# Performance work log

Hardware: AMD Instinct MI355X
Metric: run time of the kernel (lower is better)

Reference implementation:

```python
import jax, jax.numpy as jnp
import numpy as np

E = 1024; H = 16; D = E // H; L = 16
B = 4; TB = 1024; TW = 512
SCALE = D ** -0.5


def _rel_matrix(S):
    r = jnp.arange(S)
    return jnp.clip(r[None, :] - r[:, None], -L, L) + L  # [S,S] ints in [0, 2L]


def _heads(x):
    # [T, b, E] -> [b*H, T, D]
    T, b, _ = x.shape
    return x.reshape(T, b * H, D).transpose(1, 0, 2)


def _rel_logits(q, table, S):
    # Shaw-style relative-key logits without materializing [S,S,D] embeddings:
    # q: [n, S, D], table: [2L+1, D] -> [n, S, S]
    mat = _rel_matrix(S)                          # [S, S]
    all_r = jnp.einsum('ntd,rd->ntr', q, table)   # [n, S, 2L+1]
    return jnp.take_along_axis(all_r, mat[None, :, :], axis=2)


def setup_inputs() -> dict:
    key = jax.random.key(0)
    ks = jax.random.split(key, 10)
    s = 0.02
    w = lambda k, shape: jax.random.normal(k, shape, jnp.float32) * s
    return {
        'query_bpe': jax.random.normal(ks[0], (TB, B, E), jnp.float32),
        'query_word': jax.random.normal(ks[1], (TW, B, E), jnp.float32),
        'mapping': jax.random.uniform(ks[2], (B, TB, TW), jnp.float32),
        'Wq_bpe': w(ks[3], (E, E)), 'bq_bpe': jnp.zeros((E,), jnp.float32),
        'Wk_bpe': w(ks[4], (E, E)), 'bk_bpe': jnp.zeros((E,), jnp.float32),
        'Wq_word': w(ks[5], (E, E)), 'bq_word': jnp.zeros((E,), jnp.float32),
        'Wk_word': w(ks[6], (E, E)), 'bk_word': jnp.zeros((E,), jnp.float32),
        'Wv': w(ks[7], (E, E)), 'bv': jnp.zeros((E,), jnp.float32),
        'Wo': w(ks[8], (E, E)), 'bo': jnp.zeros((E,), jnp.float32),
        'rel_keys_bpe': w(ks[9], (2 * L + 1, D)),
    }


def reference(query_bpe, query_word, mapping, Wq_bpe, bq_bpe, Wk_bpe, bk_bpe,
              Wq_word, bq_word, Wk_word, bk_word, Wv, bv, Wo, bo, rel_keys_bpe):
    b = query_bpe.shape[1]
    q_bpe = _heads((query_bpe @ Wq_bpe.T + bq_bpe) * SCALE)    # [bH, TB, D]
    k_bpe = _heads(query_bpe @ Wk_bpe.T + bk_bpe)
    q_word = _heads((query_word @ Wq_word.T + bq_word) * SCALE)  # [bH, TW, D]
    k_word = _heads(query_word @ Wk_word.T + bk_word)
    v = _heads(query_bpe @ Wv.T + bv)
    # content + relative-position logits for both streams
    # (k_only path in source looks up relative_position_keys_bpe for BOTH streams)
    attn_bpe = q_bpe @ k_bpe.transpose(0, 2, 1) + _rel_logits(q_bpe, rel_keys_bpe, TB)
    attn_word = q_word @ k_word.transpose(0, 2, 1) + _rel_logits(q_word, rel_keys_bpe, TW)
    aw = attn_word.reshape(b, H, TW, TW)
    # fuse word-level scores into BPE positions via alignment mapping: M A M^T
    fused = jnp.einsum('bqw,bhws->bhqs', mapping, aw)
    fused = jnp.einsum('bhqs,bks->bhqk', fused, mapping)
    attn = attn_bpe.reshape(b, H, TB, TB) + fused
    probs = jax.nn.softmax(attn, axis=-1)
    out = jnp.einsum('bhqk,bhkd->bhqd', probs, v.reshape(b, H, TB, D))
    out = out.transpose(2, 0, 1, 3).reshape(TB, b, E)  # back to [T, B, E]
    return out @ Wo.T + bo
```

## Files before the change

kernel.cpp:

```cpp
#include <hip/hip_runtime.h>


#define DEV __device__ __forceinline__
#define GAS(x) ((const __attribute__((address_space(1))) unsigned*)(x))
#define LAS(x) ((__attribute__((address_space(3))) unsigned*)(x))

typedef unsigned short u16;
typedef __attribute__((ext_vector_type(8))) short short8;
typedef __attribute__((ext_vector_type(8))) _Float16 half8;
typedef __attribute__((ext_vector_type(4))) float floatx4;

DEV float bf2f(u16 u) { union { unsigned u; float f; } v; v.u = ((unsigned)u) << 16; return v.f; }
DEV u16 f2bf(float f) {
  union { float f; unsigned u; } v; v.f = f;
  unsigned r = v.u + 0x7FFFu + ((v.u >> 16) & 1u);
  return (u16)(r >> 16);
}
DEV u16 f2h_bits(float f) { union { _Float16 h; u16 u; } v; v.h = (_Float16)f; return v.u; }

template <int N> DEV void vmwait() {
  asm volatile("s_waitcnt vmcnt(%0)" ::"n"(N) : "memory");
  __builtin_amdgcn_sched_barrier(0);
}
DEV void barrier_raw() {
// ... 117 lines not shown
  if (i >= a.n8[z]) return;
  const float* s = a.src[z] + (size_t)i * 8;
  union { short8 v; u16 u[8]; } o;
#pragma unroll
  for (int j = 0; j < 8; ++j) o.u[j] = f2bf(s[j]);
  *(short8*)(a.dst[z] + (size_t)i * 8) = o.v;
}

struct CvtS { const float* src[3]; u16* dh[3]; u16* dl[3]; int n8[3]; };
__global__ __launch_bounds__(256) void cvt_split_kernel(CvtS a) {
  int z = blockIdx.z;
  int i = blockIdx.x * 256 + threadIdx.x;
  if (i >= a.n8[z]) return;
  const float* s = a.src[z] + (size_t)i * 8;
  union { short8 v; u16 u[8]; } oh, ol;
#pragma unroll
  for (int j = 0; j < 8; ++j) {
    float f = s[j];
    u16 h = f2bf(f);
    oh.u[j] = h;
    ol.u[j] = f2bf(f - bf2f(h));
  }
  *(short8*)(a.dh[z] + (size_t)i * 8) = oh.v;
  *(short8*)(a.dl[z] + (size_t)i * 8) = ol.v;
}

struct PAll {
  const float* Xf[5]; const float* Wf[5];
  const u16* Xh[5]; const u16* Xl[5]; const u16* Wh[5]; const u16* Wl[5];
  const float* bias[5]; float scale[5];
  u16* dh[5]; u16* dl[5]; int T[5]; int md[5]; int prep;
};

__global__ __launch_bounds__(256) void proj_all_kernel(PAll a) {
  const int z = blockIdx.z;
  const int T = a.T[z];
  if ((int)blockIdx.y >= (T >> 5)) return;
  __shared__ __align__(16) u16 LB[8][4096];
  const int tid = threadIdx.x;
  const int lane = tid & 63, wv = tid >> 6, wr = wv >> 1, wc = wv & 1;
  const int m = lane & 15, quad = lane >> 4;
  const int md = a.md[z], prep = a.prep;
  const int bx = blockIdx.x, by = blockIdx.y;
  const size_t arow = (size_t)by * 128 * 1024;
  const size_t brow = (size_t)bx * 128 * 1024;
  floatx4 acc[4][4];
  acc_zero(acc);
  if (prep) {
    const u16* Xh = a.Xh[z]; const u16* Xl = a.Xl[z];
    const u16* Wh = a.Wh[z]; const u16* Wl = a.Wl[z];
    if (md == 2) {
      stage_u16(Xh + arow, 1024, LB[0], tid);
      stage_u16(Wh + brow, 1024, LB[1], tid);
      stage_u16(Xl + arow, 1024, LB[2], tid);
      stage_u16(Wl + brow, 1024, LB[3], tid);
      for (int k0 = 0; k0 < 1024; k0 += 32) {
        int o = ((k0 >> 5) & 1) * 4;
        if (k0 + 32 < 1024) {
          int no = 4 - o;
          stage_u16(Xh + arow + k0 + 32, 1024, LB[no], tid);
          stage_u16(Wh + brow + k0 + 32, 1024, LB[no + 1], tid);
          stage_u16(Xl + arow + k0 + 32, 1024, LB[no + 2], tid);
          stage_u16(Wl + brow + k0 + 32, 1024, LB[no + 3], tid);
          vmwait<8>();
        } else vmwait<0>();
        barrier_raw();
        mma_split(LB[o], LB[o + 2], LB[o + 1], LB[o + 3], wr, wc, m, quad, acc);
        barrier_raw();
      }
    } else {
      stage_u16(Xh + arow, 1024, LB[0], tid);
      stage_u16(Wh + brow, 1024, LB[1], tid);
      for (int k0 = 0; k0 < 1024; k0 += 32) {
        int o = ((k0 >> 5) & 1) * 2;
        if (k0 + 32 < 1024) {
          int no = 2 - o;
          stage_u16(Xh + arow + k0 + 32, 1024, LB[no], tid);
          stage_u16(Wh + brow + k0 + 32, 1024, LB[no + 1], tid);
          vmwait<4>();
        } else vmwait<0>();
        barrier_raw();
        mma_bf16(LB[o], LB[o + 1], wr, wc, m, quad, acc);
        barrier_raw();
      }
    }
  } else {
    for (int k0 = 0; k0 < 1024; k0 += 32) {
      __syncthreads();
      if (md == 2) {
        stage_f32_split(a.Xf[z] + arow + k0, 1024, LB[0], LB[4], tid);
        stage_f32_split(a.Wf[z] + brow + k0, 1024, LB[2], LB[6], tid);
      } else {
        stage_f32_bf(a.Xf[z] + arow + k0, 1024, LB[0], tid);
        stage_f32_bf(a.Wf[z] + brow + k0, 1024, LB[2], tid);
      }
      __syncthreads();
      if (md == 2) mma_split(LB[0], LB[4], LB[2], LB[6], wr, wc, m, quad, acc);
      else         mma_bf16(LB[0], LB[2], wr, wc, m, quad, acc);
    }
    __syncthreads();
  }
  const float scale = a.scale[z];
  const float* bias = a.bias[z];
  u16* dh = a.dh[z];
  u16* dl = a.dl[z];
  const int row0l = wr * 64 + quad * 4;
  const int col0l = wc * 64 + m;
  if (md == 0) {
#pragma unroll
    for (int rt = 0; rt < 4; ++rt)
#pragma unroll
      for (int ct = 0; ct < 4; ++ct) {
        int col = bx * 128 + col0l + ct * 16;
        float bi = bias[col];
        int h = col >> 6, d = col & 63;
#pragma unroll
        for (int rg = 0; rg < 4; ++rg) {
          int row = by * 128 + row0l + rt * 16 + rg;
          int t = row >> 2, bb = row & 3, n = bb * 16 + h;
          float val = (acc[rt][ct][rg] + bi) * scale;
          dh[((size_t)n * T + t) * 64 + d] = f2bf(val);
        }
      }
  } else if (md == 1) {
    u16* TB = (u16*)LB;
    __syncthreads();
#pragma unroll
    for (int rt = 0; rt < 4; ++rt)
#pragma unroll
      for (int ct = 0; ct < 4; ++ct) {
        int cl = col0l + ct * 16;
        float bi = bias[bx * 128 + cl];
#pragma unroll
        for (int rg = 0; rg < 4; ++rg) {
          int rl = row0l + rt * 16 + rg;
          TB[(size_t)cl * 130 + rl] = f2bf((acc[rt][ct][rg] + bi) * scale);
        }
      }
    __syncthreads();
    for (int task = tid; task < 512; task += 256) {
      int c = task & 127, bb = task >> 7;
      int colg = bx * 128 + c, h = colg >> 6, d = colg & 63;
      size_t base = (((size_t)(bb * 16 + h)) * 64 + d) * 1024 + (size_t)by * 32;
#pragma unroll
      for (int g = 0; g < 4; ++g) {
        union { short8 v; u16 u[8]; } o;
#pragma unroll
        for (int j = 0; j < 8; ++j) o.u[j] = TB[(size_t)c * 130 + bb + 4 * (g * 8 + j)];
        *(short8*)(dh + base + g * 8) = o.v;
      }
    }
  } else {
    u16* TBh = (u16*)LB;
    u16* TBl = TBh + 64 * 130;
    for (int pass = 0; pass < 2; ++pass) {
      __syncthreads();
      if (wc == pass) {
#pragma unroll
        for (int rt = 0; rt < 4; ++rt)
#pragma unroll
          for (int ct = 0; ct < 4; ++ct) {
            int cl = ct * 16 + m;
            float bi = bias[bx * 128 + pass * 64 + cl];
#pragma unroll
            for (int rg = 0; rg < 4; ++rg) {
              int rl = row0l + rt * 16 + rg;
              float val = (acc[rt][ct][rg] + bi) * scale;
              u16 hh = f2bf(val);
              TBh[(size_t)cl * 130 + rl] = hh;
              TBl[(size_t)cl * 130 + rl] = f2bf(val - bf2f(hh));
            }
          }
      }
      __syncthreads();
      int c2 = tid & 63, bb = tid >> 6;
      int colg = bx * 128 + pass * 64 + c2, h = colg >> 6, d = colg & 63;
      size_t base = (((size_t)(bb * 16 + h)) * 64 + d) * 512 + (size_t)by * 32;
#pragma unroll
      for (int g = 0; g < 4; ++g) {
        union { short8 v; u16 u[8]; } oh, ol;
#pragma unroll
        for (int j = 0; j < 8; ++j) {
          oh.u[j] = TBh[(size_t)c2 * 130 + bb + 4 * (g * 8 + j)];
          ol.u[j] = TBl[(size_t)c2 * 130 + bb + 4 * (g * 8 + j)];
        }
        *(short8*)(dh + base + g * 8) = oh.v;
        *(short8*)(dl + base + g * 8) = ol.v;
      }
    }
  }
}

__global__ __launch_bounds__(256) void msplit_kernel(const float* __restrict__ M,
                                                     u16* __restrict__ Mh, u16* __restrict__ Ml,
                                                     u16* __restrict__ Mf) {
  int i = blockIdx.x * 256 + threadIdx.x;
  float f = M[i];
  u16 h = f2bf(f);
  Mh[i] = h;
  Ml[i] = f2bf(f - bf2f(h));
  Mf[i] = f2h_bits(f);
}

__global__ __launch_bounds__(256) void rel_bpe_kernel(const u16* __restrict__ q,
                                                      const float* __restrict__ relk,
                                                      float* __restrict__ R) {
  int nt = blockIdx.x * 256 + threadIdx.x;
  float qv[64];
#pragma unroll
  for (int c = 0; c < 8; ++c) {
    union { short8 s; u16 u[8]; } uh; uh.s = *(const short8*)(q + (size_t)nt * 64 + c * 8);
#pragma unroll
    for (int j = 0; j < 8; ++j) qv[c * 8 + j] = bf2f(uh.u[j]);
  }
  for (int r = 0; r < 33; ++r) {
    const float* krow = relk + r * 64;
    float s = 0.f;
#pragma unroll
    for (int d = 0; d < 64; ++d) s += qv[d] * krow[d];
    R[(size_t)nt * 33 + r] = s;
  }
// ... 51 lines not shown
#pragma unroll
    for (int t = 0; t < 32; ++t) {
      float a = 0.f, bb = 0.f;
#pragma unroll
      for (int c = 0; c < 2; ++c) {
        union { short8 s; _Float16 h[8]; } u;
        u.s = *(const short8*)(mrow + t * 16 + c * 8);
#pragma unroll
        for (int j = 0; j < 8; ++j) {
          int w = t * 16 + c * 8 + j;
          float mv = (float)u.h[j];
          a += mv * R[(size_t)w * 33 + 32];
          bb += mv * R[(size_t)w * 33];
        }
      }
      blkA[t] = a; blkB[t] = bb;
    }
    float run = 0.f;
#pragma unroll
    for (int i = 0; i < 33; ++i) { ps[i] = run; if (i < 32) run += blkA[i]; }
    float tot = 0.f;
#pragma unroll
    for (int i = 0; i < 32; ++i) tot += blkB[i];
    run = tot;
#pragma unroll
    for (int i = 0; i < 33; ++i) { ps[33 + i] = run; if (i < 32) run -= blkB[i]; }
  }
}

__global__ __launch_bounds__(256) void stage1band_kernel(const u16* __restrict__ Mf,
                                                         const u16* __restrict__ RT,
                                                         const float* __restrict__ PS,
                                                         u16* __restrict__ C1r, int n0) {
  __shared__ __align__(16) u16 As[2][4096], Bs[2][1024];
  const int tid = threadIdx.x, t = blockIdx.x, nl = blockIdx.z, n = n0 + nl, b = n >> 4;
  const int lane = tid & 63, wv = tid >> 6;
  const int m = lane & 15, quad = lane >> 4;
  const int w0 = (t == 0) ? 0 : (t == 15 ? 448 : 32 * t - 16);
  const size_t ma = ((size_t)b * 1024 + blockIdx.y * 128) * 512 + w0;
  const u16* rt = RT + ((size_t)nl * 16 + t) * 2048;
  stage_u16(Mf + ma, 512, As[0], tid);
  stage_u16(Mf + ma + 32, 512, As[1], tid);
  {
    int half = tid >> 7, tt = tid & 127, o = tt * 16;
    int r = o >> 6, c = (o >> 4) & 3, sc = c ^ ((r >> 1) & 3);
    __builtin_amdgcn_global_load_lds(GAS(rt + half * 32 + (size_t)r * 64 + sc * 8),
                                     LAS((char*)Bs[half] + o), 16, 0, 0);
  }
  floatx4 acc[2][2];
  floatx4 z = {0.f, 0.f, 0.f, 0.f};
  acc[0][0] = z; acc[0][1] = z; acc[1][0] = z; acc[1][1] = z;
  __syncthreads();
#pragma unroll
  for (int ks = 0; ks < 2; ++ks) {
    union { short8 s; half8 h; } af[2], bf[2];
#pragma unroll
    for (int i = 0; i < 2; ++i) af[i].s = frag_ld(As[ks], wv * 32 + i * 16 + m, quad);
#pragma unroll
    for (int i = 0; i < 2; ++i) bf[i].s = frag_ld(Bs[ks], i * 16 + m, quad);
#pragma unroll
    for (int i = 0; i < 2; ++i)
#pragma unroll
      for (int j = 0; j < 2; ++j)
        acc[i][j] = __builtin_amdgcn_mfma_f32_16x16x32_f16(af[i].h, bf[j].h, acc[i][j], 0, 0, 0);
  }
  const int ia = w0 >> 4, ib = (w0 + 64) >> 4;
  const float* ps = PS + ((size_t)nl * 1024 + blockIdx.y * 128) * 66;
#pragma unroll
  for (int i = 0; i < 2; ++i)
#pragma unroll
    for (int rg = 0; rg < 4; ++rg) {
      int row = wv * 32 + i * 16 + quad * 4 + rg;
      float ab = ps[(size_t)row * 66 + ia] + ps[(size_t)row * 66 + 33 + ib];
      int q = blockIdx.y * 128 + row;
#pragma unroll
      for (int j = 0; j < 2; ++j) {
        int s = t * 32 + j * 16 + m;
        C1r[((size_t)nl * 1024 + q) * 512 + s] = f2h_bits(acc[i][j][rg] + ab);
      }
    }
}

__global__ __launch_bounds__(256) void mqk_kernel(const u16* __restrict__ Mh, const u16* __restrict__ Ml,
                                                  const u16* __restrict__ qwTh, const u16* __restrict__ qwTl,
                                                  const u16* __restrict__ kwTh, const u16* __restrict__ kwTl,
                                                  u16* __restrict__ MQh, u16* __restrict__ MQl,
                                                  u16* __restrict__ MKh, u16* __restrict__ MKl, int n0) {
  __shared__ __align__(16) u16 LB[8][4096];
  const int tid = threadIdx.x, nl = blockIdx.y, n = n0 + nl, b = n >> 4;
  const int lane = tid & 63, wv = tid >> 6, wr = wv >> 1, wc = wv & 1;
  const int m = lane & 15, quad = lane >> 4;
  const size_t ma = ((size_t)b * 1024 + blockIdx.x * 128) * 512;
  const u16* Qh = qwTh + (size_t)n * 32768;
  const u16* Ql = qwTl + (size_t)n * 32768;
  const u16* Kh = kwTh + (size_t)n * 32768;
  const u16* Kl = kwTl + (size_t)n * 32768;
  floatx4 acc[4][4];
  acc_zero(acc);
  auto stage_set = [&](int o, int k) {
    stage_u16(Mh + ma + k, 512, LB[o], tid);
    stage_u16(Ml + ma + k, 512, LB[o + 1], tid);
    stage_u16_half(Qh + k, 512, LB[o + 2], tid, 0);
    stage_u16_half(Kh + k, 512, LB[o + 2], tid, 1);
    stage_u16_half(Ql + k, 512, LB[o + 3], tid, 0);
    stage_u16_half(Kl + k, 512, LB[o + 3], tid, 1);
  };
  stage_set(0, 0);
  for (int k0 = 0; k0 < 512; k0 += 32) {
    int o = ((k0 >> 5) & 1) * 4;
    if (k0 + 32 < 512) {
      stage_set(4 - o, k0 + 32);
      vmwait<8>();
    } else vmwait<0>();
    barrier_raw();
    mma_split(LB[o], LB[o + 1], LB[o + 2], LB[o + 3], wr, wc, m, quad, acc);
    barrier_raw();
  }
  u16* dsth = wc ? MKh : MQh;
  u16* dstl = wc ? MKl : MQl;
  const int row0 = blockIdx.x * 128 + wr * 64 + quad * 4;
#pragma unroll
  for (int rt = 0; rt < 4; ++rt)
#pragma unroll
    for (int ct = 0; ct < 4; ++ct) {
      int d = (ct * 16 + m) & 63;
#pragma unroll
      for (int rg = 0; rg < 4; ++rg) {
        int row = row0 + rt * 16 + rg;
        size_t idx = ((size_t)nl * 1024 + row) * 64 + d;
        float val = acc[rt][ct][rg];
        u16 hh = f2bf(val);
        dsth[idx] = hh;
        dstl[idx] = f2bf(val - bf2f(hh));
      }
    }
}

__global__ __launch_bounds__(256) void logits_kernel(const u16* __restrict__ qb, const u16* __restrict__ kb,
                                                     const u16* __restrict__ MQh, const u16* __restrict__ MQl,
                                                     const u16* __restrict__ MKh, const u16* __restrict__ MKl,
                                                     const u16* __restrict__ C1r, const u16* __restrict__ Mf,
                                                     const float* __restrict__ Rb, u16* __restrict__ L,
                                                     int n0) {
  __shared__ __align__(16) u16 LB[4][4096];
  const int tid = threadIdx.x, nl = blockIdx.z, n = n0 + nl, b = n >> 4;
  const int bq = blockIdx.x, bk = blockIdx.y;
  const int lane = tid & 63, wv = tid >> 6, wr = wv >> 1, wc = wv & 1;
  const int m = lane & 15, quad = lane >> 4;
  const size_t qa = ((size_t)n * 1024 + bq * 128) * 64;
  const size_t ka = ((size_t)n * 1024 + bk * 128) * 64;
  const size_t mqa = ((size_t)nl * 1024 + bq * 128) * 64;
  const size_t mka = ((size_t)nl * 1024 + bk * 128) * 64;
  const size_t ca = ((size_t)nl * 1024 + bq * 128) * 512;
  const size_t ma = ((size_t)b * 1024 + bk * 128) * 512;
  floatx4 acc[4][4];
  acc_zero(acc);
  stage_u16(qb + qa, 64, LB[0], tid);
  stage_u16(kb + ka, 64, LB[1], tid);
  __syncthreads();
  stage_u16(qb + qa + 32, 64, LB[2], tid);
  stage_u16(kb + ka + 32, 64, LB[3], tid);
  mma_bf16(LB[0], LB[1], wr, wc, m, quad, acc);
  __syncthreads();
  mma_bf16(LB[2], LB[3], wr, wc, m, quad, acc);
  __syncthreads();
#pragma unroll
  for (int k0 = 0; k0 < 64; k0 += 32) {
    stage_u16(MQh + mqa + k0, 64, LB[0], tid);
    stage_u16(MQl + mqa + k0, 64, LB[1], tid);
    stage_u16(MKh + mka + k0, 64, LB[2], tid);
    stage_u16(MKl + mka + k0, 64, LB[3], tid);
    __syncthreads();
    mma_split(LB[0], LB[1], LB[2], LB[3], wr, wc, m, quad, acc);
    __syncthreads();
  }
  stage_u16(C1r + ca, 512, LB[0], tid);
  stage_u16(Mf + ma, 512, LB[1], tid);
  for (int k0 = 0; k0 < 512; k0 += 32) {
    int o = ((k0 >> 5) & 1) * 2;
    if (k0 + 32 < 512) {
      int no = 2 - o;
      stage_u16(C1r + ca + k0 + 32, 512, LB[no], tid);
      stage_u16(Mf + ma + k0 + 32, 512, LB[no + 1], tid);
      vmwait<4>();
    } else vmwait<0>();
    barrier_raw();
    mma_f16(LB[o], LB[o + 1], wr, wc, m, quad, acc);
    barrier_raw();
  }
  const int q0 = bq * 128 + wr * 64 + quad * 4;
  const int k0c = bk * 128 + wc * 64 + m;
#pragma unroll
  for (int rt = 0; rt < 4; ++rt)
#pragma unroll
    for (int ct = 0; ct < 4; ++ct) {
      int kc = k0c + ct * 16;
#pragma unroll
      for (int rg = 0; rg < 4; ++rg) {
        int q = q0 + rt * 16 + rg;
        int id = kc - q; id = id < -16 ? -16 : (id > 16 ? 16 : id); id += 16;
        float val = acc[rt][ct][rg] + Rb[((size_t)n * 1024 + q) * 33 + id];
        L[((size_t)nl * 1024 + q) * 1024 + kc] = f2h_bits(val);
      }
    }
}

__global__ __launch_bounds__(256) void softmax_pv_kernel(const u16* __restrict__ L,
                                                         const u16* __restrict__ VT,
                                                         u16* __restrict__ AO, int n0) {
  __shared__ __align__(16) u16 Vs[2][4][2048];
  const int tid = threadIdx.x, lane = tid & 63, wv = tid >> 6;
  const int m = lane & 15, quad = lane >> 4;
  const int nl = blockIdx.y, n = n0 + nl, qt = blockIdx.x;
  const int qrow = qt * 64 + wv * 16 + m;
  const u16* Lrow = L + ((size_t)nl * 1024 + qrow) * 1024;
  const u16* Vbase = VT + (size_t)n * 64 * 1024;
  float mi = -1e30f, li = 0.f;
  floatx4 O[4];
  floatx4 z = {0.f, 0.f, 0.f, 0.f};
#pragma unroll
  for (int dt = 0; dt < 4; ++dt) O[dt] = z;

  auto stageV = [&](int kt, int buf) {
#pragma unroll
    for (int ct = 0; ct < 4; ++ct) {
      int o = tid * 16;
      int r = o >> 6, c = (o >> 4) & 3, sc = c ^ ((r >> 1) & 3);
      __builtin_amdgcn_global_load_lds(GAS(Vbase + (size_t)r * 1024 + kt * 128 + ct * 32 + sc * 8),
                                       LAS((char*)Vs[buf][ct] + o), 16, 0, 0);
    }
  };
  stageV(0, 0);
  __syncthreads();

  for (int kt = 0; kt < 8; ++kt) {
    int cur = kt & 1;
    if (kt + 1 < 8) stageV(kt + 1, cur ^ 1);

    float vals[4][8];
#pragma unroll
    for (int ct = 0; ct < 4; ++ct) {
      union { short8 s; _Float16 h[8]; } u;
      u.s = *(const short8*)(Lrow + kt * 128 + ct * 32 + quad * 8);
#pragma unroll
      for (int j = 0; j < 8; ++j) vals[ct][j] = (float)u.h[j];
    }
    float tmax = vals[0][0];
#pragma unroll
    for (int ct = 0; ct < 4; ++ct)
#pragma unroll
      for (int j = 0; j < 8; ++j) tmax = fmaxf(tmax, vals[ct][j]);
    tmax = fmaxf(tmax, __shfl_xor(tmax, 16));
    tmax = fmaxf(tmax, __shfl_xor(tmax, 32));
    float mnew = fmaxf(mi, tmax);
    float alpha = __expf(mi - mnew);
    float pv[4][8];
    float tsum = 0.f;
#pragma unroll
    for (int ct = 0; ct < 4; ++ct)
#pragma unroll
      for (int j = 0; j < 8; ++j) { pv[ct][j] = __expf(vals[ct][j] - mnew); tsum += pv[ct][j]; }
    tsum += __shfl_xor(tsum, 16);
    tsum += __shfl_xor(tsum, 32);
    li = li * alpha + tsum;
    mi = mnew;

    float ar[4];
#pragma unroll
    for (int rg = 0; rg < 4; ++rg) ar[rg] = __shfl(alpha, quad * 4 + rg);
#pragma unroll
    for (int dt = 0; dt < 4; ++dt)
#pragma unroll
      for (int rg = 0; rg < 4; ++rg) O[dt][rg] *= ar[rg];

    short8 pf[4];
#pragma unroll
    for (int ct = 0; ct < 4; ++ct) {
      union { short8 s; u16 us[8]; } up;
#pragma unroll
      for (int j = 0; j < 8; ++j) up.us[j] = f2bf(pv[ct][j]);
      pf[ct] = up.s;
    }
#pragma unroll
    for (int ct = 0; ct < 4; ++ct)
#pragma unroll
      for (int dt = 0; dt < 4; ++dt) {
        short8 vf = frag_ld(Vs[cur][ct], dt * 16 + m, quad);
        O[dt] = __builtin_amdgcn_mfma_f32_16x16x32_bf16(pf[ct], vf, O[dt], 0, 0, 0);
      }
    __syncthreads();
  }

  float linv = 1.f / li;
  float lr[4];
#pragma unroll
  for (int rg = 0; rg < 4; ++rg) lr[rg] = __shfl(linv, quad * 4 + rg);
  const int b = n >> 4, h = n & 15;
#pragma unroll
  for (int dt = 0; dt < 4; ++dt)
#pragma unroll
    for (int rg = 0; rg < 4; ++rg) {
      int q = qt * 64 + wv * 16 + quad * 4 + rg;
      float ov = O[dt][rg] * lr[rg];
      AO[((size_t)q * 4 + b) * 1024 + h * 64 + dt * 16 + m] = f2bf(ov);
    }
}

__global__ __launch_bounds__(256) void outproj_kernel(const u16* __restrict__ AO, const float* __restrict__ Wo,
                                                      const u16* __restrict__ Wob, int prep,
                                                      const float* __restrict__ bo, float* __restrict__ out) {
  __shared__ __align__(16) u16 LB[4][4096];
  const int tid = threadIdx.x;
  const int lane = tid & 63, wv = tid >> 6, wr = wv >> 1, wc = wv & 1;
  const int m = lane & 15, quad = lane >> 4;
  const u16* A = AO + (size_t)blockIdx.y * 128 * 1024;
  const size_t brow = (size_t)blockIdx.x * 128 * 1024;
  floatx4 acc[4][4];
  acc_zero(acc);
  if (prep) {
    stage_u16(A, 1024, LB[0], tid);
    stage_u16(Wob + brow, 1024, LB[1], tid);
    for (int k0 = 0; k0 < 1024; k0 += 32) {
      int o = ((k0 >> 5) & 1) * 2;
      if (k0 + 32 < 1024) {
        int no = 2 - o;
        stage_u16(A + k0 + 32, 1024, LB[no], tid);
        stage_u16(Wob + brow + k0 + 32, 1024, LB[no + 1], tid);
        vmwait<4>();
      } else vmwait<0>();
      barrier_raw();
      mma_bf16(LB[o], LB[o + 1], wr, wc, m, quad, acc);
      barrier_raw();
    }
  } else {
    for (int k0 = 0; k0 < 1024; k0 += 32) {
      __syncthreads();
      stage_u16(A + k0, 1024, LB[0], tid);
      stage_f32_bf(Wo + brow + k0, 1024, LB[2], tid);
      __syncthreads();
      mma_bf16(LB[0], LB[2], wr, wc, m, quad, acc);
    }
  }
  const int r0 = blockIdx.y * 128 + wr * 64 + quad * 4;
  const int c0 = blockIdx.x * 128 + wc * 64 + m;
#pragma unroll
  for (int rt = 0; rt < 4; ++rt)
#pragma unroll
    for (int ct = 0; ct < 4; ++ct) {
      int col = c0 + ct * 16;
      float bi = bo[col];
#pragma unroll
      for (int rg = 0; rg < 4; ++rg) {
        int row = r0 + rt * 16 + rg;
        out[(size_t)row * 1024 + col] = acc[rt][ct][rg] + bi;
      }
    }
}

extern "C" void kernel_launch(void* const* d_in, const int* in_sizes, int n_in,
                              void* d_out, int out_size, void* d_ws, size_t ws_size,
                              hipStream_t stream) {
  const float* query_bpe = (const float*)d_in[0];
  const float* query_word = (const float*)d_in[1];
  const float* mapping = (const float*)d_in[2];
  const float* Wq_bpe = (const float*)d_in[3];
  const float* bq_bpe = (const float*)d_in[4];
  const float* Wk_bpe = (const float*)d_in[5];
  const float* bk_bpe = (const float*)d_in[6];
  const float* Wq_word = (const float*)d_in[7];
  const float* bq_word = (const float*)d_in[8];
  const float* Wk_word = (const float*)d_in[9];
  const float* bk_word = (const float*)d_in[10];
  const float* Wv = (const float*)d_in[11];
  const float* bv = (const float*)d_in[12];
  const float* Wo = (const float*)d_in[13];
  const float* bo = (const float*)d_in[14];
  const float* relk = (const float*)d_in[15];
// ... 42 lines not shown
  u16* Wqw_l = (u16*)(vb + 25165824);
  u16* Wkw_h = (u16*)(vb + 27262976);
  u16* Wkw_l = (u16*)(vb + 29360128);

  if (prep) {
    CvtB cb = {};
    cb.src[0] = query_bpe; cb.dst[0] = Xb;    cb.n8[0] = 524288;
    cb.src[1] = Wq_bpe;    cb.dst[1] = Wqb;   cb.n8[1] = 131072;
    cb.src[2] = Wk_bpe;    cb.dst[2] = Wkb;   cb.n8[2] = 131072;
    cb.src[3] = Wv;        cb.dst[3] = Wvb;   cb.n8[3] = 131072;
    cb.src[4] = Wo;        cb.dst[4] = Wo_bf; cb.n8[4] = 131072;
    cvt_bf_kernel<<<dim3(2048, 1, 5), 256, 0, stream>>>(cb);
    CvtS cs = {};
    cs.src[0] = query_word; cs.dh[0] = Xw_h;  cs.dl[0] = Xw_l;  cs.n8[0] = 262144;
    cs.src[1] = Wq_word;    cs.dh[1] = Wqw_h; cs.dl[1] = Wqw_l; cs.n8[1] = 131072;
    cs.src[2] = Wk_word;    cs.dh[2] = Wkw_h; cs.dl[2] = Wkw_l; cs.n8[2] = 131072;
    cvt_split_kernel<<<dim3(1024, 1, 3), 256, 0, stream>>>(cs);
  }

  PAll pa = {};
  pa.prep = prep;
  pa.Xf[0] = query_bpe;  pa.Wf[0] = Wq_bpe;  pa.Xh[0] = Xb;   pa.Wh[0] = Wqb;
  pa.bias[0] = bq_bpe;  pa.scale[0] = 0.125f; pa.dh[0] = q_bpe; pa.T[0] = 1024; pa.md[0] = 0;
  pa.Xf[1] = query_bpe;  pa.Wf[1] = Wk_bpe;  pa.Xh[1] = Xb;   pa.Wh[1] = Wkb;
  pa.bias[1] = bk_bpe;  pa.scale[1] = 1.0f;   pa.dh[1] = k_bpe; pa.T[1] = 1024; pa.md[1] = 0;
  pa.Xf[2] = query_bpe;  pa.Wf[2] = Wv;      pa.Xh[2] = Xb;   pa.Wh[2] = Wvb;
  pa.bias[2] = bv;      pa.scale[2] = 1.0f;   pa.dh[2] = VTb;   pa.T[2] = 1024; pa.md[2] = 1;
  pa.Xf[3] = query_word; pa.Wf[3] = Wq_word; pa.Xh[3] = Xw_h; pa.Xl[3] = Xw_l;
  pa.Wh[3] = Wqw_h; pa.Wl[3] = Wqw_l;
  pa.bias[3] = bq_word; pa.scale[3] = 0.125f; pa.dh[3] = qwT_h; pa.dl[3] = qwT_l; pa.T[3] = 512; pa.md[3] = 2;
  pa.Xf[4] = query_word; pa.Wf[4] = Wk_word; pa.Xh[4] = Xw_h; pa.Xl[4] = Xw_l;
  pa.Wh[4] = Wkw_h; pa.Wl[4] = Wkw_l;
  pa.bias[4] = bk_word; pa.scale[4] = 1.0f;   pa.dh[4] = kwT_h; pa.dl[4] = kwT_l; pa.T[4] = 512; pa.md[4] = 2;
  proj_all_kernel<<<dim3(8, 32, 5), 256, 0, stream>>>(pa);

  msplit_kernel<<<dim3(4 * 1024 * 512 / 256), 256, 0, stream>>>(mapping, M_h, M_l, M_f);

  rel_bpe_kernel<<<dim3(64 * 1024 / 256), 256, 0, stream>>>(q_bpe, relk, R_bpe);
  rel_word_kernel<<<dim3(64 * 512 / 256), 256, 0, stream>>>(qwT_h, qwT_l, relk, R_word);

  for (int n0 = 0; n0 < 64; n0 += NC) {
    relprefix_kernel<<<dim3(NC * 20), 256, 0, stream>>>(R_word, M_f, RelT, PS, NC, n0);
    mqk_kernel<<<dim3(8, NC), 256, 0, stream>>>(M_h, M_l, qwT_h, qwT_l, kwT_h, kwT_l,
                                                MQh, MQl, MKh, MKl, n0);
    stage1band_kernel<<<dim3(16, 8, NC), 256, 0, stream>>>(M_f, RelT, PS, C1r, n0);
    logits_kernel<<<dim3(8, 8, NC), 256, 0, stream>>>(q_bpe, k_bpe, MQh, MQl, MKh, MKl,
                                                      C1r, M_f, R_bpe, L_c, n0);
    softmax_pv_kernel<<<dim3(16, NC), 256, 0, stream>>>(L_c, VTb, AO, n0);
  }

  outproj_kernel<<<dim3(8, 32), 256, 0, stream>>>(AO, Wo, Wo_bf, prep, bo, (float*)d_out);
}
```

Baseline: 627.1 us.

## Split projection kernel by mode, swizzle block order, pipeline V staging

Splits the fused projection kernel into a bf16-only kernel with a smaller shared-memory pool and a split-precision kernel, so the common path is not limited by the 64KB LDS allocation. The md0 epilogue now goes through an LDS transpose to make vectorized stores. Block indices are remapped in the projection, outproj and softmax kernels to group tiles for L2/XCD locality. The stage1band grid axes are swapped. In softmax_pv, the next V tile is prefetched after the softmax math with explicit waitcnt and raw barriers instead of __syncthreads. Together these aim to raise occupancy, coalesce stores and overlap loads with compute, at the cost of more complex index logic.

```diff
diff --git a/kernel.cpp b/kernel.cpp
--- a/kernel.cpp
+++ b/kernel.cpp
@@ -173,16 +173,105 @@
   u16* dh[5]; u16* dl[5]; int T[5]; int md[5]; int prep;
 };
 
-__global__ __launch_bounds__(256) void proj_all_kernel(PAll a) {
+__global__ __launch_bounds__(256) void proj_md01_kernel(PAll a) {
   const int z = blockIdx.z;
-  const int T = a.T[z];
-  if ((int)blockIdx.y >= (T >> 5)) return;
-  __shared__ __align__(16) u16 LB[8][4096];
+  __shared__ __align__(16) u16 POOL[16640];
+  auto LB = [&](int i) -> u16* { return POOL + i * 4096; };
   const int tid = threadIdx.x;
   const int lane = tid & 63, wv = tid >> 6, wr = wv >> 1, wc = wv & 1;
   const int m = lane & 15, quad = lane >> 4;
   const int md = a.md[z], prep = a.prep;
-  const int bx = blockIdx.x, by = blockIdx.y;
+  const int p = blockIdx.x + 8 * blockIdx.y;
+  const int bx = (p >> 3) & 7, by = (p & 7) + 8 * (p >> 6);
+  const size_t arow = (size_t)by * 128 * 1024;
+  const size_t brow = (size_t)bx * 128 * 1024;
+  floatx4 acc[4][4];
+  acc_zero(acc);
+  if (prep) {
+    const u16* Xh = a.Xh[z]; const u16* Wh = a.Wh[z];
+    stage_u16(Xh + arow, 1024, LB(0), tid);
+    stage_u16(Wh + brow, 1024, LB(1), tid);
+    for (int k0 = 0; k0 < 1024; k0 += 32) {
+      int o = ((k0 >> 5) & 1) * 2;
+      if (k0 + 32 < 1024) {
+        int no = 2 - o;
+        stage_u16(Xh + arow + k0 + 32, 1024, LB(no), tid);
+        stage_u16(Wh + brow + k0 + 32, 1024, LB(no + 1), tid);
+        vmwait<4>();
+      } else vmwait<0>();
+      barrier_raw();
+      mma_bf16(LB(o), LB(o + 1), wr, wc, m, quad, acc);
+      barrier_raw();
+    }
+  } else {
+    for (int k0 = 0; k0 < 1024; k0 += 32) {
+      __syncthreads();
+      stage_f32_bf(a.Xf[z] + arow + k0, 1024, LB(0), tid);
+      stage_f32_bf(a.Wf[z] + brow + k0, 1024, LB(2), tid);
+      __syncthreads();
+      mma_bf16(LB(0), LB(2), wr, wc, m, quad, acc);
+    }
+    __syncthreads();
+  }
+  const float scale = a.scale[z];
+  const float* bias = a.bias[z];
+  u16* dh = a.dh[z];
+  const int row0l = wr * 64 + quad * 4;
+  const int col0l = wc * 64 + m;
+  u16* TB = POOL;
+  __syncthreads();
+#pragma unroll
+  for (int rt = 0; rt < 4; ++rt)
+#pragma unroll
+    for (int ct = 0; ct < 4; ++ct) {
+      int cl = col0l + ct * 16;
+      float bi = bias[bx * 128 + cl];
+#pragma unroll
+      for (int rg = 0; rg < 4; ++rg) {
+        int rl = row0l + rt * 16 + rg;
+        TB[(size_t)cl * 130 + rl] = f2bf((acc[rt][ct][rg] + bi) * scale);
+      }
+    }
+  __syncthreads();
+  if (md == 0) {
+    int t_local = tid & 31, nloc = tid >> 5;
+    int bb = nloc >> 1, hl = nloc & 1;
+    int n = bb * 16 + bx * 2 + hl;
+    int rl = t_local * 4 + bb;
+    size_t base = ((size_t)n * 1024 + by * 32 + t_local) * 64;
+#pragma unroll
+    for (int g = 0; g < 8; ++g) {
+      union { short8 v; u16 u[8]; } o;
+#pragma unroll
+      for (int j = 0; j < 8; ++j) o.u[j] = TB[(size_t)(hl * 64 + g * 8 + j) * 130 + rl];
+      *(short8*)(dh + base + g * 8) = o.v;
+    }
+  } else {
+    for (int task = tid; task < 512; task += 256) {
+      int c = task & 127, bb = task >> 7;
+      int colg = bx * 128 + c, h = colg >> 6, d = colg & 63;
+      size_t base = (((size_t)(bb * 16 + h)) * 64 + d) * 1024 + (size_t)by * 32;
+#pragma unroll
+      for (int g = 0; g < 4; ++g) {
+        union { short8 v; u16 u[8]; } o;
+#pragma unroll
+        for (int j = 0; j < 8; ++j) o.u[j] = TB[(size_t)c * 130 + bb + 4 * (g * 8 + j)];
+        *(short8*)(dh + base + g * 8) = o.v;
+      }
+    }
+  }
+}
+
+__global__ __launch_bounds__(256) void proj_md2_kernel(PAll a) {
+  const int z = blockIdx.z + 3;
+  __shared__ __align__(16) u16 POOL[32768];
+  auto LB = [&](int i) -> u16* { return POOL + i * 4096; };
+  const int tid = threadIdx.x;
+  const int lane = tid & 63, wv = tid >> 6, wr = wv >> 1, wc = wv & 1;
+  const int m = lane & 15, quad = lane >> 4;
+  const int prep = a.prep;
+  const int p = blockIdx.x + 8 * blockIdx.y;
+  const int bx = (p >> 3) & 7, by = (p & 7) + 8 * (p >> 6);
   const size_t arow = (size_t)by * 128 * 1024;
   const size_t brow = (size_t)bx * 128 * 1024;
   floatx4 acc[4][4];
@@ -190,54 +279,31 @@
   if (prep) {
     const u16* Xh = a.Xh[z]; const u16* Xl = a.Xl[z];
     const u16* Wh = a.Wh[z]; const u16* Wl = a.Wl[z];
-    if (md == 2) {
-      stage_u16(Xh + arow, 1024, LB[0], tid);
-      stage_u16(Wh + brow, 1024, LB[1], tid);
-      stage_u16(Xl + arow, 1024, LB[2], tid);
-      stage_u16(Wl + brow, 1024, LB[3], tid);
-      for (int k0 = 0; k0 < 1024; k0 += 32) {
-        int o = ((k0 >> 5) & 1) * 4;
-        if (k0 + 32 < 1024) {
-          int no = 4 - o;
-          stage_u16(Xh + arow + k0 + 32, 1024, LB[no], tid);
-          stage_u16(Wh + brow + k0 + 32, 1024, LB[no + 1], tid);
-          stage_u16(Xl + arow + k0 + 32, 1024, LB[no + 2], tid);
-          stage_u16(Wl + brow + k0 + 32, 1024, LB[no + 3], tid);
-          vmwait<8>();
-        } else vmwait<0>();
-        barrier_raw();
-        mma_split(LB[o], LB[o + 2], LB[o + 1], LB[o + 3], wr, wc, m, quad, acc);
-        barrier_raw();
-      }
-    } else {
-      stage_u16(Xh + arow, 1024, LB[0], tid);
-      stage_u16(Wh + brow, 1024, LB[1], tid);
-      for (int k0 = 0; k0 < 1024; k0 += 32) {
-        int o = ((k0 >> 5) & 1) * 2;
-        if (k0 + 32 < 1024) {
-          int no = 2 - o;
-          stage_u16(Xh + arow + k0 + 32, 1024, LB[no], tid);
-          stage_u16(Wh + brow + k0 + 32, 1024, LB[no + 1], tid);
-          vmwait<4>();
-        } else vmwait<0>();
-        barrier_raw();
-        mma_bf16(LB[o], LB[o + 1], wr, wc, m, quad, acc);
-        barrier_raw();
-      }
+    stage_u16(Xh + arow, 1024, LB(0), tid);
+    stage_u16(Wh + brow, 1024, LB(1), tid);
+    stage_u16(Xl + arow, 1024, LB(2), tid);
+    stage_u16(Wl + brow, 1024, LB(3), tid);
+    for (int k0 = 0; k0 < 1024; k0 += 32) {
+      int o = ((k0 >> 5) & 1) * 4;
+      if (k0 + 32 < 1024) {
+        int no = 4 - o;
+        stage_u16(Xh + arow + k0 + 32, 1024, LB(no), tid);
+        stage_u16(Wh + brow + k0 + 32, 1024, LB(no + 1), tid);
+        stage_u16(Xl + arow + k0 + 32, 1024, LB(no + 2), tid);
+        stage_u16(Wl + brow + k0 + 32, 1024, LB(no + 3), tid);
+        vmwait<8>();
+      } else vmwait<0>();
+      barrier_raw();
+      mma_split(LB(o), LB(o + 2), LB(o + 1), LB(o + 3), wr, wc, m, quad, acc);
+      barrier_raw();
     }
   } else {
     for (int k0 = 0; k0 < 1024; k0 += 32) {
       __syncthreads();
-      if (md == 2) {
-        stage_f32_split(a.Xf[z] + arow + k0, 1024, LB[0], LB[4], tid);
-        stage_f32_split(a.Wf[z] + brow + k0, 1024, LB[2], LB[6], tid);
-      } else {
-        stage_f32_bf(a.Xf[z] + arow + k0, 1024, LB[0], tid);
-        stage_f32_bf(a.Wf[z] + brow + k0, 1024, LB[2], tid);
-      }
+      stage_f32_split(a.Xf[z] + arow + k0, 1024, LB(0), LB(4), tid);
+      stage_f32_split(a.Wf[z] + brow + k0, 1024, LB(2), LB(6), tid);
       __syncthreads();
-      if (md == 2) mma_split(LB[0], LB[4], LB[2], LB[6], wr, wc, m, quad, acc);
-      else         mma_bf16(LB[0], LB[2], wr, wc, m, quad, acc);
+      mma_split(LB(0), LB(4), LB(2), LB(6), wr, wc, m, quad, acc);
     }
     __syncthreads();
   }
@@ -246,88 +312,41 @@
   u16* dh = a.dh[z];
   u16* dl = a.dl[z];
   const int row0l = wr * 64 + quad * 4;
-  const int col0l = wc * 64 + m;
-  if (md == 0) {
-#pragma unroll
-    for (int rt = 0; rt < 4; ++rt)
-#pragma unroll
-      for (int ct = 0; ct < 4; ++ct) {
-        int col = bx * 128 + col0l + ct * 16;
-        float bi = bias[col];
-        int h = col >> 6, d = col & 63;
-#pragma unroll
-        for (int rg = 0; rg < 4; ++rg) {
-          int row = by * 128 + row0l + rt * 16 + rg;
-          int t = row >> 2, bb = row & 3, n = bb * 16 + h;
-          float val = (acc[rt][ct][rg] + bi) * scale;
-          dh[((size_t)n * T + t) * 64 + d] = f2bf(val);
+  u16* TBh = POOL;
+  u16* TBl = POOL + 64 * 130;
+  for (int pass = 0; pass < 2; ++pass) {
+    __syncthreads();
+    if (wc == pass) {
+#pragma unroll
+      for (int rt = 0; rt < 4; ++rt)
+#pragma unroll
+        for (int ct = 0; ct < 4; ++ct) {
+          int cl = ct * 16 + m;
+          float bi = bias[bx * 128 + pass * 64 + cl];
+#pragma unroll
+          for (int rg = 0; rg < 4; ++rg) {
+            int rl = row0l + rt * 16 + rg;
+            float val = (acc[rt][ct][rg] + bi) * scale;
+            u16 hh = f2bf(val);
+            TBh[(size_t)cl * 130 + rl] = hh;
+            TBl[(size_t)cl * 130 + rl] = f2bf(val - bf2f(hh));
+          }
         }
+    }
+    __syncthreads();
+    int c2 = tid & 63, bb = tid >> 6;
+    int colg = bx * 128 + pass * 64 + c2, h = colg >> 6, d = colg & 63;
+    size_t base = (((size_t)(bb * 16 + h)) * 64 + d) * 512 + (size_t)by * 32;
+#pragma unroll
+    for (int g = 0; g < 4; ++g) {
+      union { short8 v; u16 u[8]; } oh, ol;
+#pragma unroll
+      for (int j = 0; j < 8; ++j) {
+        oh.u[j] = TBh[(size_t)c2 * 130 + bb + 4 * (g * 8 + j)];
+        ol.u[j] = TBl[(size_t)c2 * 130 + bb + 4 * (g * 8 + j)];
       }
-  } else if (md == 1) {
-    u16* TB = (u16*)LB;
-    __syncthreads();
-#pragma unroll
-    for (int rt = 0; rt < 4; ++rt)
-#pragma unroll
-      for (int ct = 0; ct < 4; ++ct) {
-        int cl = col0l + ct * 16;
-        float bi = bias[bx * 128 + cl];
-#pragma unroll
-        for (int rg = 0; rg < 4; ++rg) {
-          int rl = row0l + rt * 16 + rg;
-          TB[(size_t)cl * 130 + rl] = f2bf((acc[rt][ct][rg] + bi) * scale);
-        }
-      }
-    __syncthreads();
-    for (int task = tid; task < 512; task += 256) {
-      int c = task & 127, bb = task >> 7;
-      int colg = bx * 128 + c, h = colg >> 6, d = colg & 63;
-      size_t base = (((size_t)(bb * 16 + h)) * 64 + d) * 1024 + (size_t)by * 32;
-#pragma unroll
-      for (int g = 0; g < 4; ++g) {
-        union { short8 v; u16 u[8]; } o;
-#pragma unroll
-        for (int j = 0; j < 8; ++j) o.u[j] = TB[(size_t)c * 130 + bb + 4 * (g * 8 + j)];
-        *(short8*)(dh + base + g * 8) = o.v;
-      }
-    }
-  } else {
-    u16* TBh = (u16*)LB;
-    u16* TBl = TBh + 64 * 130;
-    for (int pass = 0; pass < 2; ++pass) {
-      __syncthreads();
-      if (wc == pass) {
-#pragma unroll
-        for (int rt = 0; rt < 4; ++rt)
-#pragma unroll
-          for (int ct = 0; ct < 4; ++ct) {
-            int cl = ct * 16 + m;
-            float bi = bias[bx * 128 + pass * 64 + cl];
-#pragma unroll
-            for (int rg = 0; rg < 4; ++rg) {
-              int rl = row0l + rt * 16 + rg;
-              float val = (acc[rt][ct][rg] + bi) * scale;
-              u16 hh = f2bf(val);
-              TBh[(size_t)cl * 130 + rl] = hh;
-              TBl[(size_t)cl * 130 + rl] = f2bf(val - bf2f(hh));
-            }
-          }
-      }
-      __syncthreads();
-      int c2 = tid & 63, bb = tid >> 6;
-      int colg = bx * 128 + pass * 64 + c2, h = colg >> 6, d = colg & 63;
-      size_t base = (((size_t)(bb * 16 + h)) * 64 + d) * 512 + (size_t)by * 32;
-#pragma unroll
-      for (int g = 0; g < 4; ++g) {
-        union { short8 v; u16 u[8]; } oh, ol;
-#pragma unroll
-        for (int j = 0; j < 8; ++j) {
-          oh.u[j] = TBh[(size_t)c2 * 130 + bb + 4 * (g * 8 + j)];
-          ol.u[j] = TBl[(size_t)c2 * 130 + bb + 4 * (g * 8 + j)];
-        }
-        *(short8*)(dh + base + g * 8) = oh.v;
-        *(short8*)(dl + base + g * 8) = ol.v;
-      }
+      *(short8*)(dh + base + g * 8) = oh.v;
+      *(short8*)(dl + base + g * 8) = ol.v;
     }
   }
 }
@@ -445,20 +464,22 @@
                                                          const u16* __restrict__ RT,
                                                          const float* __restrict__ PS,
                                                          u16* __restrict__ C1r, int n0) {
-  __shared__ __align__(16) u16 As[2][4096], Bs[2][1024];
-  const int tid = threadIdx.x, t = blockIdx.x, nl = blockIdx.z, n = n0 + nl, b = n >> 4;
+  __shared__ __align__(16) u16 As0[4096], As1[4096], Bs0[1024], Bs1[1024];
+  const int tid = threadIdx.x, qy = blockIdx.x, t = blockIdx.y;
+  const int nl = blockIdx.z, n = n0 + nl, b = n >> 4;
   const int lane = tid & 63, wv = tid >> 6;
   const int m = lane & 15, quad = lane >> 4;
   const int w0 = (t == 0) ? 0 : (t == 15 ? 448 : 32 * t - 16);
-  const size_t ma = ((size_t)b * 1024 + blockIdx.y * 128) * 512 + w0;
+  const size_t ma = ((size_t)b * 1024 + qy * 128) * 512 + w0;
   const u16* rt = RT + ((size_t)nl * 16 + t) * 2048;
-  stage_u16(Mf + ma, 512, As[0], tid);
-  stage_u16(Mf + ma + 32, 512, As[1], tid);
+  stage_u16(Mf + ma, 512, As0, tid);
+  stage_u16(Mf + ma + 32, 512, As1, tid);
   {
     int half = tid >> 7, tt = tid & 127, o = tt * 16;
     int r = o >> 6, c = (o >> 4) & 3, sc = c ^ ((r >> 1) & 3);
+    u16* bs = half ? Bs1 : Bs0;
     __builtin_amdgcn_global_load_lds(GAS(rt + half * 32 + (size_t)r * 64 + sc * 8),
-                                     LAS((char*)Bs[half] + o), 16, 0, 0);
+                                     LAS((char*)bs + o), 16, 0, 0);
   }
   floatx4 acc[2][2];
   floatx4 z = {0.f, 0.f, 0.f, 0.f};
@@ -466,11 +487,13 @@
   __syncthreads();
 #pragma unroll
   for (int ks = 0; ks < 2; ++ks) {
+    const u16* As = ks ? As1 : As0;
+    const u16* Bs = ks ? Bs1 : Bs0;
     union { short8 s; half8 h; } af[2], bf[2];
 #pragma unroll
-    for (int i = 0; i < 2; ++i) af[i].s = frag_ld(As[ks], wv * 32 + i * 16 + m, quad);
-#pragma unroll
-    for (int i = 0; i < 2; ++i) bf[i].s = frag_ld(Bs[ks], i * 16 + m, quad);
+    for (int i = 0; i < 2; ++i) af[i].s = frag_ld(As, wv * 32 + i * 16 + m, quad);
+#pragma unroll
+    for (int i = 0; i < 2; ++i) bf[i].s = frag_ld(Bs, i * 16 + m, quad);
 #pragma unroll
     for (int i = 0; i < 2; ++i)
 #pragma unroll
@@ -478,14 +501,14 @@
         acc[i][j] = __builtin_amdgcn_mfma_f32_16x16x32_f16(af[i].h, bf[j].h, acc[i][j], 0, 0, 0);
   }
   const int ia = w0 >> 4, ib = (w0 + 64) >> 4;
-  const float* ps = PS + ((size_t)nl * 1024 + blockIdx.y * 128) * 66;
+  const float* ps = PS + ((size_t)nl * 1024 + qy * 128) * 66;
 #pragma unroll
   for (int i = 0; i < 2; ++i)
 #pragma unroll
     for (int rg = 0; rg < 4; ++rg) {
       int row = wv * 32 + i * 16 + quad * 4 + rg;
       float ab = ps[(size_t)row * 66 + ia] + ps[(size_t)row * 66 + 33 + ib];
-      int q = blockIdx.y * 128 + row;
+      int q = qy * 128 + row;
 #pragma unroll
       for (int j = 0; j < 2; ++j) {
         int s = t * 32 + j * 16 + m;
@@ -499,7 +522,8 @@
                                                   const u16* __restrict__ kwTh, const u16* __restrict__ kwTl,
                                                   u16* __restrict__ MQh, u16* __restrict__ MQl,
                                                   u16* __restrict__ MKh, u16* __restrict__ MKl, int n0) {
-  __shared__ __align__(16) u16 LB[8][4096];
+  __shared__ __align__(16) u16 POOL[32768];
+  auto LB = [&](int i) -> u16* { return POOL + i * 4096; };
   const int tid = threadIdx.x, nl = blockIdx.y, n = n0 + nl, b = n >> 4;
   const int lane = tid & 63, wv = tid >> 6, wr = wv >> 1, wc = wv & 1;
   const int m = lane & 15, quad = lane >> 4;
@@ -511,12 +535,12 @@
   floatx4 acc[4][4];
   acc_zero(acc);
   auto stage_set = [&](int o, int k) {
-    stage_u16(Mh + ma + k, 512, LB[o], tid);
-    stage_u16(Ml + ma + k, 512, LB[o + 1], tid);
-    stage_u16_half(Qh + k, 512, LB[o + 2], tid, 0);
-    stage_u16_half(Kh + k, 512, LB[o + 2], tid, 1);
-    stage_u16_half(Ql + k, 512, LB[o + 3], tid, 0);
-    stage_u16_half(Kl + k, 512, LB[o + 3], tid, 1);
+    stage_u16(Mh + ma + k, 512, LB(o), tid);
+    stage_u16(Ml + ma + k, 512, LB(o + 1), tid);
+    stage_u16_half(Qh + k, 512, LB(o + 2), tid, 0);
+    stage_u16_half(Kh + k, 512, LB(o + 2), tid, 1);
+    stage_u16_half(Ql + k, 512, LB(o + 3), tid, 0);
+    stage_u16_half(Kl + k, 512, LB(o + 3), tid, 1);
   };
   stage_set(0, 0);
   for (int k0 = 0; k0 < 512; k0 += 32) {
@@ -526,7 +550,7 @@
       vmwait<8>();
     } else vmwait<0>();
     barrier_raw();
-    mma_split(LB[o], LB[o + 1], LB[o + 2], LB[o + 3], wr, wc, m, quad, acc);
+    mma_split(LB(o), LB(o + 1), LB(o + 2), LB(o + 3), wr, wc, m, quad, acc);
     barrier_raw();
   }
   u16* dsth = wc ? MKh : MQh;
@@ -555,7 +579,8 @@
                                                      const u16* __restrict__ C1r, const u16* __restrict__ Mf,
                                                      const float* __restrict__ Rb, u16* __restrict__ L,
                                                      int n0) {
-  __shared__ __align__(16) u16 LB[4][4096];
+  __shared__ __align__(16) u16 POOL[16384];
+  auto LB = [&](int i) -> u16* { return POOL + i * 4096; };
   const int tid = threadIdx.x, nl = blockIdx.z, n = n0 + nl, b = n >> 4;
   const int bq = blockIdx.x, bk = blockIdx.y;
   const int lane = tid & 63, wv = tid >> 6, wr = wv >> 1, wc = wv & 1;
@@ -568,37 +593,37 @@
   const size_t ma = ((size_t)b * 1024 + bk * 128) * 512;
   floatx4 acc[4][4];
   acc_zero(acc);
-  stage_u16(qb + qa, 64, LB[0], tid);
-  stage_u16(kb + ka, 64, LB[1], tid);
+  stage_u16(qb + qa, 64, LB(0), tid);
+  stage_u16(kb + ka, 64, LB(1), tid);
   __syncthreads();
-  stage_u16(qb + qa + 32, 64, LB[2], tid);
-  stage_u16(kb + ka + 32, 64, LB[3], tid);
-  mma_bf16(LB[0], LB[1], wr, wc, m, quad, acc);
+  stage_u16(qb + qa + 32, 64, LB(2), tid);
+  stage_u16(kb + ka + 32, 64, LB(3), tid);
+  mma_bf16(LB(0), LB(1), wr, wc, m, quad, acc);
   __syncthreads();
-  mma_bf16(LB[2], LB[3], wr, wc, m, quad, acc);
+  mma_bf16(LB(2), LB(3), wr, wc, m, quad, acc);
   __syncthreads();
 #pragma unroll
   for (int k0 = 0; k0 < 64; k0 += 32) {
-    stage_u16(MQh + mqa + k0, 64, LB[0], tid);
-    stage_u16(MQl + mqa + k0, 64, LB[1], tid);
-    stage_u16(MKh + mka + k0, 64, LB[2], tid);
-    stage_u16(MKl + mka + k0, 64, LB[3], tid);
+    stage_u16(MQh + mqa + k0, 64, LB(0), tid);
+    stage_u16(MQl + mqa + k0, 64, LB(1), tid);
+    stage_u16(MKh + mka + k0, 64, LB(2), tid);
+    stage_u16(MKl + mka + k0, 64, LB(3), tid);
     __syncthreads();
-    mma_split(LB[0], LB[1], LB[2], LB[3], wr, wc, m, quad, acc);
+    mma_split(LB(0), LB(1), LB(2), LB(3), wr, wc, m, quad, acc);
     __syncthreads();
   }
-  stage_u16(C1r + ca, 512, LB[0], tid);
-  stage_u16(Mf + ma, 512, LB[1], tid);
+  stage_u16(C1r + ca, 512, LB(0), tid);
+  stage_u16(Mf + ma, 512, LB(1), tid);
   for (int k0 = 0; k0 < 512; k0 += 32) {
     int o = ((k0 >> 5) & 1) * 2;
     if (k0 + 32 < 512) {
       int no = 2 - o;
-      stage_u16(C1r + ca + k0 + 32, 512, LB[no], tid);
-      stage_u16(Mf + ma + k0 + 32, 512, LB[no + 1], tid);
+      stage_u16(C1r + ca + k0 + 32, 512, LB(no), tid);
+      stage_u16(Mf + ma + k0 + 32, 512, LB(no + 1), tid);
       vmwait<4>();
     } else vmwait<0>();
     barrier_raw();
-    mma_f16(LB[o], LB[o + 1], wr, wc, m, quad, acc);
+    mma_f16(LB(o), LB(o + 1), wr, wc, m, quad, acc);
     barrier_raw();
   }
   const int q0 = bq * 128 + wr * 64 + quad * 4;
@@ -620,11 +645,18 @@
 
 __global__ __launch_bounds__(256) void softmax_pv_kernel(const u16* __restrict__ L,
                                                          const u16* __restrict__ VT,
-                                                         u16* __restrict__ AO, int n0) {
+                                                         u16* __restrict__ AO, int NCk, int n0) {
   __shared__ __align__(16) u16 Vs[2][4][2048];
   const int tid = threadIdx.x, lane = tid & 63, wv = tid >> 6;
   const int m = lane & 15, quad = lane >> 4;
-  const int nl = blockIdx.y, n = n0 + nl, qt = blockIdx.x;
+  int qt, nl;
+  if (NCk >= 8) {
+    int lin = blockIdx.x + 16 * blockIdx.y;
+    int xcd = lin & 7, j = lin >> 3;
+    qt = j & 15;
+    nl = xcd + 8 * (j >> 4);
+  } else { qt = blockIdx.x; nl = blockIdx.y; }
+  const int n = n0 + nl;
   const int qrow = qt * 64 + wv * 16 + m;
   const u16* Lrow = L + ((size_t)nl * 1024 + qrow) * 1024;
   const u16* Vbase = VT + (size_t)n * 64 * 1024;
@@ -644,11 +676,9 @@
     }
   };
   stageV(0, 0);
-  __syncthreads();
 
   for (int kt = 0; kt < 8; ++kt) {
     int cur = kt & 1;
-    if (kt + 1 < 8) stageV(kt + 1, cur ^ 1);
 
     float vals[4][8];
 #pragma unroll
@@ -678,6 +708,10 @@
     li = li * alpha + tsum;
     mi = mnew;
 
+    if (kt + 1 < 8) { stageV(kt + 1, cur ^ 1); vmwait<4>(); }
+    else vmwait<0>();
+    barrier_raw();
+
     float ar[4];
 #pragma unroll
     for (int rg = 0; rg < 4; ++rg) ar[rg] = __shfl(alpha, quad * 4 + rg);
@@ -701,7 +735,7 @@
         short8 vf = frag_ld(Vs[cur][ct], dt * 16 + m, quad);
         O[dt] = __builtin_amdgcn_mfma_f32_16x16x32_bf16(pf[ct], vf, O[dt], 0, 0, 0);
       }
-    __syncthreads();
+    barrier_raw();
   }
 
   float linv = 1.f / li;
@@ -722,40 +756,43 @@
 __global__ __launch_bounds__(256) void outproj_kernel(const u16* __restrict__ AO, const float* __restrict__ Wo,
                                                       const u16* __restrict__ Wob, int prep,
                                                       const float* __restrict__ bo, float* __restrict__ out) {
-  __shared__ __align__(16) u16 LB[4][4096];
+  __shared__ __align__(16) u16 POOL[16384];
+  auto LB = [&](int i) -> u16* { return POOL + i * 4096; };
   const int tid = threadIdx.x;
   const int lane = tid & 63, wv = tid >> 6, wr = wv >> 1, wc = wv & 1;
   const int m = lane & 15, quad = lane >> 4;
-  const u16* A = AO + (size_t)blockIdx.y * 128 * 1024;
-  const size_t brow = (size_t)blockIdx.x * 128 * 1024;
+  const int p = blockIdx.x + 8 * blockIdx.y;
+  const int bx = (p >> 3) & 7, by = (p & 7) + 8 * (p >> 6);
+  const u16* A = AO + (size_t)by * 128 * 1024;
+  const size_t brow = (size_t)bx * 128 * 1024;
   floatx4 acc[4][4];
   acc_zero(acc);
   if (prep) {
-    stage_u16(A, 1024, LB[0], tid);
-    stage_u16(Wob + brow, 1024, LB[1], tid);
+    stage_u16(A, 1024, LB(0), tid);
+    stage_u16(Wob + brow, 1024, LB(1), tid);
     for (int k0 = 0; k0 < 1024; k0 += 32) {
       int o = ((k0 >> 5) & 1) * 2;
       if (k0 + 32 < 1024) {
         int no = 2 - o;
-        stage_u16(A + k0 + 32, 1024, LB[no], tid);
-        stage_u16(Wob + brow + k0 + 32, 1024, LB[no + 1], tid);
+        stage_u16(A + k0 + 32, 1024, LB(no), tid);
+        stage_u16(Wob + brow + k0 + 32, 1024, LB(no + 1), tid);
         vmwait<4>();
       } else vmwait<0>();
       barrier_raw();
-      mma_bf16(LB[o], LB[o + 1], wr, wc, m, quad, acc);
+      mma_bf16(LB(o), LB(o + 1), wr, wc, m, quad, acc);
       barrier_raw();
     }
   } else {
     for (int k0 = 0; k0 < 1024; k0 += 32) {
       __syncthreads();
-      stage_u16(A + k0, 1024, LB[0], tid);
-      stage_f32_bf(Wo + brow + k0, 1024, LB[2], tid);
+      stage_u16(A + k0, 1024, LB(0), tid);
+      stage_f32_bf(Wo + brow + k0, 1024, LB(2), tid);
       __syncthreads();
-      mma_bf16(LB[0], LB[2], wr, wc, m, quad, acc);
-    }
-  }
-  const int r0 = blockIdx.y * 128 + wr * 64 + quad * 4;
-  const int c0 = blockIdx.x * 128 + wc * 64 + m;
+      mma_bf16(LB(0), LB(2), wr, wc, m, quad, acc);
+    }
+  }
+  const int r0 = by * 128 + wr * 64 + quad * 4;
+  const int c0 = bx * 128 + wc * 64 + m;
 #pragma unroll
   for (int rt = 0; rt < 4; ++rt)
 #pragma unroll
@@ -864,7 +901,8 @@
   pa.Xf[4] = query_word; pa.Wf[4] = Wk_word; pa.Xh[4] = Xw_h; pa.Xl[4] = Xw_l;
   pa.Wh[4] = Wkw_h; pa.Wl[4] = Wkw_l;
   pa.bias[4] = bk_word; pa.scale[4] = 1.0f;   pa.dh[4] = kwT_h; pa.dl[4] = kwT_l; pa.T[4] = 512; pa.md[4] = 2;
-  proj_all_kernel<<<dim3(8, 32, 5), 256, 0, stream>>>(pa);
+  proj_md01_kernel<<<dim3(8, 32, 3), 256, 0, stream>>>(pa);
+  proj_md2_kernel<<<dim3(8, 16, 2), 256, 0, stream>>>(pa);
 
   msplit_kernel<<<dim3(4 * 1024 * 512 / 256), 256, 0, stream>>>(mapping, M_h, M_l, M_f);
 
@@ -875,10 +913,10 @@
     relprefix_kernel<<<dim3(NC * 20), 256, 0, stream>>>(R_word, M_f, RelT, PS, NC, n0);
     mqk_kernel<<<dim3(8, NC), 256, 0, stream>>>(M_h, M_l, qwT_h, qwT_l, kwT_h, kwT_l,
                                                 MQh, MQl, MKh, MKl, n0);
-    stage1band_kernel<<<dim3(16, 8, NC), 256, 0, stream>>>(M_f, RelT, PS, C1r, n0);
+    stage1band_kernel<<<dim3(8, 16, NC), 256, 0, stream>>>(M_f, RelT, PS, C1r, n0);
     logits_kernel<<<dim3(8, 8, NC), 256, 0, stream>>>(q_bpe, k_bpe, MQh, MQl, MKh, MKl,
                                                       C1r, M_f, R_bpe, L_c, n0);
-    softmax_pv_kernel<<<dim3(16, NC), 256, 0, stream>>>(L_c, VTb, AO, n0);
+    softmax_pv_kernel<<<dim3(16, NC), 256, 0, stream>>>(L_c, VTb, AO, NC, n0);
   }
 
   outproj_kernel<<<dim3(8, 32), 256, 0, stream>>>(AO, Wo, Wo_bf, prep, bo, (float*)d_out);
```

Result: faster. 596.8 us (-4.8%).
